# Kernel tuning notes

Hardware: AMD Instinct MI355X
Metric: run time of the kernel (lower is better)

Reference implementation:

```python
import jax, jax.numpy as jnp
import numpy as np

N_ENTITY = 100000
N_RELATION = 64
DIM = 16
N_HOP = 2
N_MEM = 32
N_NODES = 16384


def setup_inputs() -> dict:
    key = jax.random.key(0)
    ks = jax.random.split(key, 7)
    return {
        "nodes": jax.random.randint(ks[0], (N_NODES,), 0, N_ENTITY),
        "memories_h": jax.random.randint(ks[1], (N_HOP, N_NODES, N_MEM), 0, N_ENTITY),
        "memories_r": jax.random.randint(ks[2], (N_HOP, N_NODES, N_MEM), 0, N_RELATION),
        "memories_t": jax.random.randint(ks[3], (N_HOP, N_NODES, N_MEM), 0, N_ENTITY),
        "entity_emb": jax.random.normal(ks[4], (N_ENTITY, DIM), jnp.float32) * 0.1,
        "relation_emb": jax.random.normal(ks[5], (N_RELATION, DIM * DIM), jnp.float32) * 0.1,
        "W": jax.random.normal(ks[6], (DIM, DIM), jnp.float32) * 0.1,
    }


def reference(nodes, memories_h, memories_r, memories_t, entity_emb, relation_emb, W):
    # item embeddings for the query nodes: [N, D]
    item = entity_emb[nodes]
    o_list = []
    for hop in range(N_HOP):  # small fixed hop count (2)
        h = entity_emb[memories_h[hop]]                                  # [N, M, D]
        r = relation_emb[memories_r[hop]].reshape(-1, N_MEM, DIM, DIM)   # [N, M, D, D]
        t = entity_emb[memories_t[hop]]                                  # [N, M, D]
        # Rh = R @ h : [N, M, D]
        Rh = jnp.einsum('nmde,nme->nmd', r, h)
        # attention over the n_memory slots (softmax dim=0 per node in original)
        probs = jax.nn.softmax(jnp.einsum('nmd,nd->nm', Rh, item), axis=1)
        # weighted sum of tails: [N, D]
        o = jnp.einsum('nm,nmd->nd', probs, t)
        # item_update_mode == 'plus_transform': Linear(dim, dim, bias=False)
        item = (item + o) @ W.T
        o_list.append(o)
    # Faithful to the original torch in-place semantics: at hop 0 the line
    # `kg_feature += o_list[0]` doubles o0 in place; the final result for
    # n_hop=2 is therefore o1 + 2*o0.
    return o_list[1] + 2.0 * o_list[0]
```

## Files before the change

kernel.cpp:

```cpp
#include <hip/hip_runtime.h>

#define NE     100000
#define NR     64
#define DIM    16
#define NHOP   2
#define NMEM   32
#define NNODES 16384

#define COLP   24
#define RELP   392
#define WPITCH 20

static __device__ __forceinline__ int sdot4(unsigned a, unsigned b, int c) {
#if __has_builtin(__builtin_amdgcn_sdot4)
    return __builtin_amdgcn_sdot4((int)a, (int)b, c, false);
#else
    #pragma unroll
    for (int k = 0; k < 4; ++k) {
        int xa = (int)((a >> (8 * k)) & 0xffu); xa = (xa ^ 0x80) - 0x80;
        int xb = (int)((b >> (8 * k)) & 0xffu); xb = (xb ^ 0x80) - 0x80;
        c += xa * xb;
    }
    return c;
#endif
}

static __device__ __forceinline__ float dpp_sum16(float v) {
    union { int i; float f; } a, b;
    a.f = v;
    b.i = __builtin_amdgcn_update_dpp(0, a.i, 0xB1,  0xf, 0xf, true); a.f += b.f;
    b.i = __builtin_amdgcn_update_dpp(0, a.i, 0x4E,  0xf, 0xf, true); a.f += b.f;
    b.i = __builtin_amdgcn_update_dpp(0, a.i, 0x124, 0xf, 0xf, true); a.f += b.f;
    b.i = __builtin_amdgcn_update_dpp(0, a.i, 0x128, 0xf, 0xf, true); a.f += b.f;
    return a.f;
}
static __device__ __forceinline__ float dpp_max16(float v) {
    union { int i; float f; } a, b;
    a.f = v;
    b.i = __builtin_amdgcn_update_dpp(0, a.i, 0xB1,  0xf, 0xf, true); a.f = fmaxf(a.f, b.f);
    b.i = __builtin_amdgcn_update_dpp(0, a.i, 0x4E,  0xf, 0xf, true); a.f = fmaxf(a.f, b.f);
    b.i = __builtin_amdgcn_update_dpp(0, a.i, 0x124, 0xf, 0xf, true); a.f = fmaxf(a.f, b.f);
    b.i = __builtin_amdgcn_update_dpp(0, a.i, 0x128, 0xf, 0xf, true); a.f = fmaxf(a.f, b.f);
    return a.f;
}

static __device__ __forceinline__ float bcast(float v, int l) {
    return __int_as_float(__builtin_amdgcn_readlane(__float_as_int(v), l));
}

extern "C" __global__ void __launch_bounds__(512, 8)
ripple_kernel(const int* __restrict__ nodes,
              const int* __restrict__ mh,
              const int* __restrict__ mr,
              const int* __restrict__ mt,
              const float* __restrict__ ent,
              const float* __restrict__ rel,
              const float* __restrict__ W,
              float* __restrict__ out)
{
    __shared__ __align__(16) char  rt[NR * RELP];
    __shared__ __align__(16) float ws[DIM * WPITCH + 8];

    const int tid = threadIdx.x;

    float vbuf[32];
    {
        float m = 0.f;
        #pragma unroll
        for (int i = 0; i < 8; ++i) {
            int T = i * 512 + tid;
            int r = T >> 6, e = (T >> 2) & 15, d0 = (T & 3) << 2;
            const float* p = rel + r * 256 + d0 * 16 + e;
            float a = p[0], b = p[16], c = p[32], d = p[48];
            vbuf[4 * i + 0] = a; vbuf[4 * i + 1] = b;
            vbuf[4 * i + 2] = c; vbuf[4 * i + 3] = d;
            m = fmaxf(m, fmaxf(fmaxf(fabsf(a), fabsf(b)), fmaxf(fabsf(c), fabsf(d))));
        }
        #pragma unroll
        for (int off = 32; off; off >>= 1) m = fmaxf(m, __shfl_xor(m, off));
        if ((tid & 63) == 0) ws[DIM * WPITCH + (tid >> 6)] = m;
        if (tid < 256) ws[(tid >> 4) * WPITCH + (tid & 15)] = W[tid];
    }
    __syncthreads();

    float smax;
    {
        float m = 1e-30f;
        #pragma unroll
        for (int j = 0; j < 8; ++j) m = fmaxf(m, ws[DIM * WPITCH + j]);
        smax = m;
    }
    const float rs = smax * (1.f / 127.f);

    {
        const float qs = 127.f / smax;
        #pragma unroll
        for (int i = 0; i < 8; ++i) {
            int T = i * 512 + tid;
            int r = T >> 6, e = (T >> 2) & 15, d0 = (T & 3) << 2;
            unsigned pk = 0;
            #pragma unroll
            for (int j = 0; j < 4; ++j) {
                int q = (int)rintf(vbuf[4 * i + j] * qs);
                q = q < -127 ? -127 : (q > 127 ? 127 : q);
                pk |= ((unsigned)q & 0xffu) << (8 * j);
            }
            *(unsigned*)&rt[r * RELP + e * COLP + d0] = pk;
        }
    }
    __syncthreads();

    const int lane = tid & 63;
    const int wid  = tid >> 6;
    const int g    = lane >> 4;
    const int e    = lane & 15;
    const int n    = blockIdx.x * 8 + wid;

    float item    = ent[nodes[n] * DIM + e];
    float out_acc = 0.f;

    #pragma unroll
    for (int hop = 0; hop < NHOP; ++hop) {
        const float mx  = fmaxf(dpp_max16(fabsf(item)), 1e-30f);
        int q8 = (int)rintf(item * (127.f / mx));
        q8 = q8 < -127 ? -127 : (q8 > 127 ? 127 : q8);
        unsigned ip[4];
        #pragma unroll
        for (int j = 0; j < 4; ++j) {
            unsigned b0 = (unsigned)__builtin_amdgcn_readlane(q8, 4 * j + 0) & 0xffu;
            unsigned b1 = (unsigned)__builtin_amdgcn_readlane(q8, 4 * j + 1) & 0xffu;
            unsigned b2 = (unsigned)__builtin_amdgcn_readlane(q8, 4 * j + 2) & 0xffu;
            unsigned b3 = (unsigned)__builtin_amdgcn_readlane(q8, 4 * j + 3) & 0xffu;
            ip[j] = b0 | (b1 << 8) | (b2 << 16) | (b3 << 24);
        }
        const float cq = rs * mx * (1.f / 127.f);

        const int ibase = hop * (NNODES * NMEM) + n * NMEM + g * 8;
        int hi[8], ri[8], ti[8];
        {
            const int4* p;
            p = (const int4*)(mh + ibase); *(int4*)&hi[0] = p[0]; *(int4*)&hi[4] = p[1];
            p = (const int4*)(mr + ibase); *(int4*)&ri[0] = p[0]; *(int4*)&ri[4] = p[1];
            p = (const int4*)(mt + ibase); *(int4*)&ti[0] = p[0]; *(int4*)&ti[4] = p[1];
        }

        float Z = 0.f, o = 0.f;
        #pragma unroll
        for (int it = 0; it < 8; ++it) {
            const char* cb = rt + ri[it] * RELP + e * COLP;
            uint2 u0 = *(const uint2*)cb;
            uint2 u1 = *(const uint2*)(cb + 8);
            int acc = sdot4(u1.y, ip[3],
                      sdot4(u1.x, ip[2],
                      sdot4(u0.y, ip[1],
                      sdot4(u0.x, ip[0], 0))));
            float hv = ent[hi[it] * DIM + e];
            float sc = dpp_sum16((float)acc * cq * hv);
            float ex = __expf(sc);
            float tv = ent[ti[it] * DIM + e];
            Z += ex;
            o += ex * tv;
        }
        Z += __shfl_xor(Z, 16);
        Z += __shfl_xor(Z, 32);
        o += __shfl_xor(o, 16);
        o += __shfl_xor(o, 32);
        o *= 1.f / Z;

        out_acc += (hop == 0) ? 2.f * o : o;

        const float v = item + o;
        float nit = 0.f;
        const float4* wr = (const float4*)&ws[e * WPITCH];
        #pragma unroll
        for (int j = 0; j < 4; ++j) {
            float4 w = wr[j];
            nit += w.x * bcast(v, 4 * j + 0) + w.y * bcast(v, 4 * j + 1)
                 + w.z * bcast(v, 4 * j + 2) + w.w * bcast(v, 4 * j + 3);
        }
        item = nit;
    }

    if (lane < 16) out[n * DIM + e] = out_acc;
}

extern "C" void kernel_launch(void* const* d_in, const int* in_sizes, int n_in,
                              void* d_out, int out_size, void* d_ws, size_t ws_size,
                              hipStream_t stream) {
    const int*   nodes = (const int*)d_in[0];
    const int*   mh    = (const int*)d_in[1];
    const int*   mr    = (const int*)d_in[2];
    const int*   mt    = (const int*)d_in[3];
    const float* ent   = (const float*)d_in[4];
    const float* rel   = (const float*)d_in[5];
    const float* W     = (const float*)d_in[6];
    float*       out   = (float*)d_out;

    dim3 grid(NNODES / 8);
    dim3 block(512);
    ripple_kernel<<<grid, block, 0, stream>>>(nodes, mh, mr, mt, ent, rel, W, out);
}
```

Before: 104.2 us.

## Shrink blocks to 256 threads, compact int8 relation table, hoist head-embedding loads

Blocks now have 256 threads and handle 4 nodes each, with twice as many blocks. The shared int8 relation table drops its padded column pitch for a dense 16-byte stride, cutting LDS footprint per block. The max-abs pass now reads relation rows as float4 instead of keeping values in registers, and the quantize pass reloads them from global memory. All head-embedding gathers are issued before the attention loop to raise memory-level parallelism. Each block still rebuilds the whole relation table, so doubling the block count doubles that setup work, and the dense stride may cause LDS bank conflicts.

```diff
diff --git a/kernel.cpp b/kernel.cpp
--- a/kernel.cpp
+++ b/kernel.cpp
@@ -7,9 +7,9 @@
 #define NMEM   32
 #define NNODES 16384
 
-#define COLP   24
-#define RELP   392
+#define RELP   272
 #define WPITCH 20
+#define WSMAX  (DIM * WPITCH)
 
 static __device__ __forceinline__ int sdot4(unsigned a, unsigned b, int c) {
 #if __has_builtin(__builtin_amdgcn_sdot4)
@@ -48,7 +48,7 @@
     return __int_as_float(__builtin_amdgcn_readlane(__float_as_int(v), l));
 }
 
-extern "C" __global__ void __launch_bounds__(512, 8)
+extern "C" __global__ void __launch_bounds__(256, 6)
 ripple_kernel(const int* __restrict__ nodes,
               const int* __restrict__ mh,
               const int* __restrict__ mr,
@@ -59,53 +59,47 @@
               float* __restrict__ out)
 {
     __shared__ __align__(16) char  rt[NR * RELP];
-    __shared__ __align__(16) float ws[DIM * WPITCH + 8];
+    __shared__ __align__(16) float ws[WSMAX + 4];
 
     const int tid = threadIdx.x;
 
-    float vbuf[32];
     {
+        const float4* rel4 = (const float4*)rel;
         float m = 0.f;
         #pragma unroll
-        for (int i = 0; i < 8; ++i) {
-            int T = i * 512 + tid;
-            int r = T >> 6, e = (T >> 2) & 15, d0 = (T & 3) << 2;
-            const float* p = rel + r * 256 + d0 * 16 + e;
-            float a = p[0], b = p[16], c = p[32], d = p[48];
-            vbuf[4 * i + 0] = a; vbuf[4 * i + 1] = b;
-            vbuf[4 * i + 2] = c; vbuf[4 * i + 3] = d;
-            m = fmaxf(m, fmaxf(fmaxf(fabsf(a), fabsf(b)), fmaxf(fabsf(c), fabsf(d))));
+        for (int i = 0; i < 16; ++i) {
+            float4 v = rel4[i * 256 + tid];
+            m = fmaxf(m, fmaxf(fmaxf(fabsf(v.x), fabsf(v.y)),
+                               fmaxf(fabsf(v.z), fabsf(v.w))));
         }
         #pragma unroll
         for (int off = 32; off; off >>= 1) m = fmaxf(m, __shfl_xor(m, off));
-        if ((tid & 63) == 0) ws[DIM * WPITCH + (tid >> 6)] = m;
-        if (tid < 256) ws[(tid >> 4) * WPITCH + (tid & 15)] = W[tid];
+        if ((tid & 63) == 0) ws[WSMAX + (tid >> 6)] = m;
+        ws[(tid >> 4) * WPITCH + (tid & 15)] = W[tid];
     }
     __syncthreads();
 
-    float smax;
-    {
-        float m = 1e-30f;
-        #pragma unroll
-        for (int j = 0; j < 8; ++j) m = fmaxf(m, ws[DIM * WPITCH + j]);
-        smax = m;
-    }
+    const float smax = fmaxf(fmaxf(fmaxf(ws[WSMAX], ws[WSMAX + 1]),
+                                   fmaxf(ws[WSMAX + 2], ws[WSMAX + 3])), 1e-30f);
     const float rs = smax * (1.f / 127.f);
 
     {
         const float qs = 127.f / smax;
         #pragma unroll
-        for (int i = 0; i < 8; ++i) {
-            int T = i * 512 + tid;
+        for (int i = 0; i < 16; ++i) {
+            int T = i * 256 + tid;
             int r = T >> 6, e = (T >> 2) & 15, d0 = (T & 3) << 2;
-            unsigned pk = 0;
-            #pragma unroll
-            for (int j = 0; j < 4; ++j) {
-                int q = (int)rintf(vbuf[4 * i + j] * qs);
-                q = q < -127 ? -127 : (q > 127 ? 127 : q);
-                pk |= ((unsigned)q & 0xffu) << (8 * j);
-            }
-            *(unsigned*)&rt[r * RELP + e * COLP + d0] = pk;
+            const float* p = rel + r * 256 + d0 * 16 + e;
+            float a = p[0], b = p[16], c = p[32], d = p[48];
+            int qa = (int)rintf(a * qs), qb = (int)rintf(b * qs);
+            int qc = (int)rintf(c * qs), qd = (int)rintf(d * qs);
+            qa = qa < -127 ? -127 : (qa > 127 ? 127 : qa);
+            qb = qb < -127 ? -127 : (qb > 127 ? 127 : qb);
+            qc = qc < -127 ? -127 : (qc > 127 ? 127 : qc);
+            qd = qd < -127 ? -127 : (qd > 127 ? 127 : qd);
+            unsigned pk = ((unsigned)qa & 0xffu)        | (((unsigned)qb & 0xffu) << 8)
+                        | (((unsigned)qc & 0xffu) << 16) | (((unsigned)qd & 0xffu) << 24);
+            *(unsigned*)&rt[r * RELP + e * 16 + d0] = pk;
         }
     }
     __syncthreads();
@@ -114,14 +108,14 @@
     const int wid  = tid >> 6;
     const int g    = lane >> 4;
     const int e    = lane & 15;
-    const int n    = blockIdx.x * 8 + wid;
+    const int n    = blockIdx.x * 4 + wid;
 
     float item    = ent[nodes[n] * DIM + e];
     float out_acc = 0.f;
 
     #pragma unroll
     for (int hop = 0; hop < NHOP; ++hop) {
-        const float mx  = fmaxf(dpp_max16(fabsf(item)), 1e-30f);
+        const float mx = fmaxf(dpp_max16(fabsf(item)), 1e-30f);
         int q8 = (int)rintf(item * (127.f / mx));
         q8 = q8 < -127 ? -127 : (q8 > 127 ? 127 : q8);
         unsigned ip[4];
@@ -144,20 +138,23 @@
             p = (const int4*)(mt + ibase); *(int4*)&ti[0] = p[0]; *(int4*)&ti[4] = p[1];
         }
 
+        float hv[8];
+        #pragma unroll
+        for (int it = 0; it < 8; ++it) hv[it] = ent[hi[it] * DIM + e];
+
         float Z = 0.f, o = 0.f;
         #pragma unroll
         for (int it = 0; it < 8; ++it) {
-            const char* cb = rt + ri[it] * RELP + e * COLP;
+            float tv = ent[ti[it] * DIM + e];
+            const char* cb = rt + ri[it] * RELP + e * 16;
             uint2 u0 = *(const uint2*)cb;
             uint2 u1 = *(const uint2*)(cb + 8);
             int acc = sdot4(u1.y, ip[3],
                       sdot4(u1.x, ip[2],
                       sdot4(u0.y, ip[1],
                       sdot4(u0.x, ip[0], 0))));
-            float hv = ent[hi[it] * DIM + e];
-            float sc = dpp_sum16((float)acc * cq * hv);
+            float sc = dpp_sum16((float)acc * cq * hv[it]);
             float ex = __expf(sc);
-            float tv = ent[ti[it] * DIM + e];
             Z += ex;
             o += ex * tv;
         }
@@ -196,7 +193,7 @@
     const float* W     = (const float*)d_in[6];
     float*       out   = (float*)d_out;
 
-    dim3 grid(NNODES / 8);
-    dim3 block(512);
+    dim3 grid(NNODES / 4);
+    dim3 block(256);
     ripple_kernel<<<grid, block, 0, stream>>>(nodes, mh, mr, mt, ent, rel, W, out);
 }
```

Result: slower. 126.5 us (+21.3%).
